# Kernel optimization log

Hardware: AMD Instinct MI355X
Metric: run time of the kernel (lower is better)

Reference implementation:

```python
import jax, jax.numpy as jnp
import numpy as np

B, C, H, W = 32, 3, 512, 512


def _make_rot(N):
    k = np.arange(N, dtype=np.float64)[None, :] * np.pi / (2 * N)
    return jnp.asarray(np.cos(k), jnp.float32), jnp.asarray(np.sin(k), jnp.float32)


def setup_inputs() -> dict:
    key = jax.random.key(0)
    X = jax.random.normal(key, (B, C, H, W), dtype=jnp.float32)
    W_r_weight, W_i_weight = _make_rot(W)
    W_r_height, W_i_height = _make_rot(H)
    return {
        "X": X,
        "W_r_weight": W_r_weight,
        "W_i_weight": W_i_weight,
        "W_r_height": W_r_height,
        "W_i_height": W_i_height,
    }


def _idct1(X, W_r, W_i):
    # 1D IDCT (DCT-III) along last axis via irfft, norm='ortho'.
    shp = X.shape
    N = shp[-1]
    Xv = X.reshape(-1, N) * 0.5
    # ortho scaling: col 0 -> *sqrt(N)*2, cols 1: -> *sqrt(N/2)*2 (after the /2)
    col_scale = np.full((N,), np.sqrt(N / 2) * 2, dtype=np.float32)
    col_scale[0] = np.sqrt(N) * 2
    Xv = Xv * jnp.asarray(col_scale)
    # V_t_i[:, 0] = 0; V_t_i[:, j] = -Xv[:, N-j] for j >= 1
    Vti = jnp.concatenate([jnp.zeros_like(Xv[:, :1]), -Xv[:, :0:-1]], axis=1)
    Vr = Xv * W_r - Vti * W_i
    Vi = Xv * W_i + Vti * W_r
    v = jnp.fft.irfft(jax.lax.complex(Vr, Vi), n=N, axis=1)  # [M, N] real
    # de-interleave: even outputs from front half, odd outputs from reversed tail
    x = jnp.zeros_like(v)
    x = x.at[:, ::2].set(v[:, : N - N // 2])
    x = x.at[:, 1::2].set(v[:, ::-1][:, : N // 2])
    return x.reshape(shp)


def reference(X, W_r_weight, W_i_weight, W_r_height, W_i_height):
    x = _idct1(X, W_r_weight, W_i_weight)          # IDCT over width
    x = jnp.swapaxes(x, -1, -2)
    x = _idct1(x, W_r_height, W_i_height)          # IDCT over height
    return jnp.swapaxes(x, -1, -2)
```

## Files before the change

kernel.cpp:

```cpp
#include <hip/hip_runtime.h>
#include <math.h>
#include <stdint.h>

#define N512 512

typedef __attribute__((ext_vector_type(8))) short short8;
typedef __attribute__((ext_vector_type(4))) float floatx4;

__device__ __forceinline__ short f2bf(float f) {
    uint32_t u = __float_as_uint(f);
    uint32_t r = u + 0x7fffu + ((u >> 16) & 1u);
    return (short)(r >> 16);
}

__device__ __forceinline__ short f2bf_fast(float f) {
    return (short)((__float_as_uint(f) + 0x8000u) >> 16);
}

__device__ __forceinline__ void gload_lds16(const void* g, void* l) {
    __builtin_amdgcn_global_load_lds(
        (const __attribute__((address_space(1))) void*)g,
        (__attribute__((address_space(3))) void*)l,
        16, 0, 0);
}

__global__ __launch_bounds__(256) void build_idct_matrix_bf16(short* __restrict__ M) {
    int idx = blockIdx.x * 256 + threadIdx.x;
    int n = idx >> 9;
    int k = idx & 511;
    int j = (k * (2 * n + 1)) & (4 * N512 - 1);
    float theta = (float)j * (3.14159265358979323846f / (2.0f * (float)N512));
    float s = (k == 0) ? 0.044194173824159216f : 0.0625f;
    M[idx] = f2bf(s * cosf(theta));
}

__global__ __launch_bounds__(256) void gemm_s1(const short* __restrict__ A,
                                               const float* __restrict__ Xg,
                                               short* __restrict__ Tg) {
    __shared__ short lds[2 * 8192];
    short* ldsA = lds;
    short* ldsB = lds + 8192;

    const int t = threadIdx.x;
    const int w = t >> 6;
    const int l = t & 63;
    const int q = (t >> 4) & 3;
    const int r = t & 15;

    const int bm0 = blockIdx.y * 128;
    const int bn0 = blockIdx.x * 128;
    const int wm0 = (w >> 1) * 64;
    const int wn0 = (w & 1) * 64;

    const float* Xs = Xg + ((long)blockIdx.z << 18);
    short* Tt = Tg + ((long)blockIdx.z << 18);

    const int rsub = l >> 3;
    const int glog = (l & 7) ^ rsub;

    const int brow = t >> 4;
    const int col4 = t & 15;
    const int bg   = col4 >> 1;
    const int bh   = col4 & 1;

    floatx4 acc[4][4] = {};

    for (int kt = 0; kt < 8; ++kt) {
        const int k0 = kt * 64;
#pragma unroll
        for (int i = 0; i < 4; ++i) {
            const int chunk = w * 4 + i;
            const int rt = chunk * 8 + rsub;
            gload_lds16(A + (((long)(bm0 + rt)) << 9) + k0 + glog * 8,
                        ldsA + chunk * 512);
        }
        {
            float4 v[8];
#pragma unroll
            for (int p = 0; p < 8; ++p) {
                const int rt = p * 16 + brow;
                v[p] = *(const float4*)(Xs + (((long)(bn0 + rt)) << 9) + k0 + col4 * 4);
            }
#pragma unroll
            for (int p = 0; p < 8; ++p) {
                const int rt = p * 16 + brow;
                const int bchunk = rt >> 3;
                const int brs = rt & 7;
                short4 o;
                o.x = f2bf_fast(v[p].x);
                o.y = f2bf_fast(v[p].y);
                o.z = f2bf_fast(v[p].z);
                o.w = f2bf_fast(v[p].w);
                *(short4*)(ldsB + bchunk * 512 + brs * 64 + ((bg ^ brs) * 8) + bh * 4) = o;
            }
        }
        __syncthreads();
#pragma unroll
        for (int kk = 0; kk < 2; ++kk) {
            const int c = kk * 4 + q;
            const int goff = ((c ^ (r & 7)) * 8);
            short8 af[4], bf[4];
#pragma unroll
            for (int i = 0; i < 4; ++i) {
                af[i] = *(const short8*)(ldsA + (wm0 + i * 16 + r) * 64 + goff);
                bf[i] = *(const short8*)(ldsB + (wn0 + i * 16 + r) * 64 + goff);
            }
#pragma unroll
            for (int i = 0; i < 4; ++i)
#pragma unroll
                for (int j = 0; j < 4; ++j)
                    acc[i][j] = __builtin_amdgcn_mfma_f32_16x16x32_bf16(
                        af[i], bf[j], acc[i][j], 0, 0, 0);
        }
        __syncthreads();
    }

#pragma unroll
    for (int i = 0; i < 4; ++i) {
        const int mrow = bm0 + wm0 + i * 16 + q * 4;
#pragma unroll
        for (int j = 0; j < 4; ++j) {
            const int ncol = bn0 + wn0 + j * 16 + r;
#pragma unroll
            for (int rg = 0; rg < 4; ++rg)
                Tt[(long)(mrow + rg) * N512 + ncol] = f2bf(acc[i][j][rg]);
        }
    }
}

__global__ __launch_bounds__(256) void gemm_s2(const short* __restrict__ A,
                                               const short* __restrict__ Bg,
                                               float* __restrict__ Cg) {
    __shared__ short lds[2 * 8192];
    short* ldsA = lds;
    short* ldsB = lds + 8192;

    const int t = threadIdx.x;
    const int w = t >> 6;
    const int l = t & 63;
    const int q = (t >> 4) & 3;
    const int r = t & 15;

    const int bm0 = blockIdx.y * 128;
    const int bn0 = blockIdx.x * 128;
    const int wm0 = (w >> 1) * 64;
    const int wn0 = (w & 1) * 64;

    const short* Bs = Bg + ((long)blockIdx.z << 18);
    float* C = Cg + ((long)blockIdx.z << 18);

    const int rsub = l >> 3;
    const int glog = (l & 7) ^ rsub;

    floatx4 acc[4][4] = {};

    for (int kt = 0; kt < 8; ++kt) {
        const int k0 = kt * 64;
#pragma unroll
        for (int i = 0; i < 4; ++i) {
            const int chunk = w * 4 + i;
            const int rt = chunk * 8 + rsub;
            gload_lds16(A + (((long)(bm0 + rt)) << 9) + k0 + glog * 8,
                        ldsA + chunk * 512);
            gload_lds16(Bs + (((long)(bn0 + rt)) << 9) + k0 + glog * 8,
                        ldsB + chunk * 512);
        }
        __syncthreads();
#pragma unroll
        for (int kk = 0; kk < 2; ++kk) {
            const int c = kk * 4 + q;
            const int goff = ((c ^ (r & 7)) * 8);
            short8 af[4], bf[4];
#pragma unroll
            for (int i = 0; i < 4; ++i) {
                af[i] = *(const short8*)(ldsA + (wm0 + i * 16 + r) * 64 + goff);
                bf[i] = *(const short8*)(ldsB + (wn0 + i * 16 + r) * 64 + goff);
            }
#pragma unroll
            for (int i = 0; i < 4; ++i)
#pragma unroll
                for (int j = 0; j < 4; ++j)
                    acc[i][j] = __builtin_amdgcn_mfma_f32_16x16x32_bf16(
                        af[i], bf[j], acc[i][j], 0, 0, 0);
        }
        __syncthreads();
    }

#pragma unroll
    for (int i = 0; i < 4; ++i) {
        const int mrow = bm0 + wm0 + i * 16 + q * 4;
#pragma unroll
        for (int j = 0; j < 4; ++j) {
            const int ncol = bn0 + wn0 + j * 16 + r;
#pragma unroll
            for (int rg = 0; rg < 4; ++rg)
                C[(long)(mrow + rg) * N512 + ncol] = acc[i][j][rg];
        }
    }
}

extern "C" void kernel_launch(void* const* d_in, const int* in_sizes, int n_in,
                              void* d_out, int out_size, void* d_ws, size_t ws_size,
                              hipStream_t stream) {
    const float* X = (const float*)d_in[0];
    float* out = (float*)d_out;

    const long plane = (long)N512 * N512;
    const int slices = in_sizes[0] / (int)plane;

    short* Mb = (short*)d_ws;
    short* Tt = Mb + plane;

    long avail = (long)ws_size - plane * 2;
    int chunk = (int)(avail / (plane * 2));
    if (chunk > slices) chunk = slices;
    if (chunk < 1) chunk = 1;

    build_idct_matrix_bf16<<<dim3((int)(plane / 256)), dim3(256), 0, stream>>>(Mb);

    for (int s0 = 0; s0 < slices; s0 += chunk) {
        int c = (s0 + chunk <= slices) ? chunk : (slices - s0);
        gemm_s1<<<dim3(4, 4, c), dim3(256), 0, stream>>>(
            Mb, X + (long)s0 * plane, Tt);
        gemm_s2<<<dim3(4, 4, c), dim3(256), 0, stream>>>(
            Mb, Tt, out + (long)s0 * plane);
    }
}
```

Baseline: 237.9 us.

## Double-buffer LDS tiles with explicit vmcnt waits in both GEMM stages

Both GEMM kernels now keep two LDS buffers and prefetch the next K-tile (global-to-LDS loads, plus register loads for the fp32 X tile in stage 1) while MFMAs run on the current tile. Hand-placed s_waitcnt vmcnt/lgkmcnt and raw barriers replace __syncthreads so loads stay in flight across compute. LDS use doubles to 64KB per block, which may cut occupancy. The host also rounds the slice chunk count down to a multiple of 32.

```diff
diff --git a/kernel.cpp b/kernel.cpp
--- a/kernel.cpp
+++ b/kernel.cpp
@@ -6,6 +6,11 @@
 
 typedef __attribute__((ext_vector_type(8))) short short8;
 typedef __attribute__((ext_vector_type(4))) float floatx4;
+
+#define VMCNT(n) asm volatile("s_waitcnt vmcnt(" #n ")" ::: "memory")
+#define LGKM0    asm volatile("s_waitcnt lgkmcnt(0)" ::: "memory")
+#define FENCE    asm volatile("" ::: "memory")
+#define BARRIER  __builtin_amdgcn_s_barrier()
 
 __device__ __forceinline__ short f2bf(float f) {
     uint32_t u = __float_as_uint(f);
@@ -37,9 +42,7 @@
 __global__ __launch_bounds__(256) void gemm_s1(const short* __restrict__ A,
                                                const float* __restrict__ Xg,
                                                short* __restrict__ Tg) {
-    __shared__ short lds[2 * 8192];
-    short* ldsA = lds;
-    short* ldsB = lds + 8192;
+    __shared__ __align__(16) short lds[4 * 8192];
 
     const int t = threadIdx.x;
     const int w = t >> 6;
@@ -64,23 +67,87 @@
     const int bh   = col4 & 1;
 
     floatx4 acc[4][4] = {};
+    float4 v[8];
+
+#pragma unroll
+    for (int p = 0; p < 8; ++p) {
+        const int rt = p * 16 + brow;
+        v[p] = *(const float4*)(Xs + (((long)(bn0 + rt)) << 9) + col4 * 4);
+    }
+#pragma unroll
+    for (int i = 0; i < 4; ++i) {
+        const int chunk = w * 4 + i;
+        const int rt = chunk * 8 + rsub;
+        gload_lds16(A + (((long)(bm0 + rt)) << 9) + glog * 8,
+                    lds + chunk * 512);
+    }
+    VMCNT(4);
+#pragma unroll
+    for (int p = 0; p < 8; ++p) {
+        const int rt = p * 16 + brow;
+        const int bchunk = rt >> 3;
+        const int brs = rt & 7;
+        short4 o;
+        o.x = f2bf_fast(v[p].x);
+        o.y = f2bf_fast(v[p].y);
+        o.z = f2bf_fast(v[p].z);
+        o.w = f2bf_fast(v[p].w);
+        *(short4*)(lds + 8192 + bchunk * 512 + brs * 64 + ((bg ^ brs) * 8) + bh * 4) = o;
+    }
+    LGKM0;
 
     for (int kt = 0; kt < 8; ++kt) {
-        const int k0 = kt * 64;
-#pragma unroll
-        for (int i = 0; i < 4; ++i) {
-            const int chunk = w * 4 + i;
-            const int rt = chunk * 8 + rsub;
-            gload_lds16(A + (((long)(bm0 + rt)) << 9) + k0 + glog * 8,
-                        ldsA + chunk * 512);
-        }
-        {
-            float4 v[8];
+        short* bufc = lds + (kt & 1) * 16384;
+        short* bufn = lds + ((kt + 1) & 1) * 16384;
+
+        if (kt < 7) {
+            const int k0n = (kt + 1) * 64;
 #pragma unroll
             for (int p = 0; p < 8; ++p) {
                 const int rt = p * 16 + brow;
-                v[p] = *(const float4*)(Xs + (((long)(bn0 + rt)) << 9) + k0 + col4 * 4);
-            }
+                v[p] = *(const float4*)(Xs + (((long)(bn0 + rt)) << 9) + k0n + col4 * 4);
+            }
+#pragma unroll
+            for (int i = 0; i < 4; ++i) {
+                const int chunk = w * 4 + i;
+                const int rt = chunk * 8 + rsub;
+                gload_lds16(A + (((long)(bm0 + rt)) << 9) + k0n + glog * 8,
+                            bufn + chunk * 512);
+            }
+            VMCNT(12);
+        } else {
+            VMCNT(0);
+        }
+        BARRIER;
+        FENCE;
+
+        {
+            short* ldsA = bufc;
+            short* ldsB = bufc + 8192;
+#pragma unroll
+            for (int kk = 0; kk < 2; ++kk) {
+                const int c = kk * 4 + q;
+                const int goff = ((c ^ (r & 7)) * 8);
+                short8 af[4], bfr[4];
+#pragma unroll
+                for (int i = 0; i < 4; ++i) {
+                    af[i]  = *(const short8*)(ldsA + (wm0 + i * 16 + r) * 64 + goff);
+                    bfr[i] = *(const short8*)(ldsB + (wn0 + i * 16 + r) * 64 + goff);
+                }
+#pragma unroll
+                for (int i = 0; i < 4; ++i)
+#pragma unroll
+                    for (int j = 0; j < 4; ++j)
+                        acc[i][j] = __builtin_amdgcn_mfma_f32_16x16x32_bf16(
+                            af[i], bfr[j], acc[i][j], 0, 0, 0);
+            }
+        }
+
+        FENCE;
+        BARRIER;
+
+        if (kt < 7) {
+            VMCNT(4);
 #pragma unroll
             for (int p = 0; p < 8; ++p) {
                 const int rt = p * 16 + brow;
@@ -91,28 +158,10 @@
                 o.y = f2bf_fast(v[p].y);
                 o.z = f2bf_fast(v[p].z);
                 o.w = f2bf_fast(v[p].w);
-                *(short4*)(ldsB + bchunk * 512 + brs * 64 + ((bg ^ brs) * 8) + bh * 4) = o;
-            }
-        }
-        __syncthreads();
-#pragma unroll
-        for (int kk = 0; kk < 2; ++kk) {
-            const int c = kk * 4 + q;
-            const int goff = ((c ^ (r & 7)) * 8);
-            short8 af[4], bf[4];
-#pragma unroll
-            for (int i = 0; i < 4; ++i) {
-                af[i] = *(const short8*)(ldsA + (wm0 + i * 16 + r) * 64 + goff);
-                bf[i] = *(const short8*)(ldsB + (wn0 + i * 16 + r) * 64 + goff);
-            }
-#pragma unroll
-            for (int i = 0; i < 4; ++i)
-#pragma unroll
-                for (int j = 0; j < 4; ++j)
-                    acc[i][j] = __builtin_amdgcn_mfma_f32_16x16x32_bf16(
-                        af[i], bf[j], acc[i][j], 0, 0, 0);
-        }
-        __syncthreads();
+                *(short4*)(bufn + 8192 + bchunk * 512 + brs * 64 + ((bg ^ brs) * 8) + bh * 4) = o;
+            }
+            LGKM0;
+        }
     }
 
 #pragma unroll
@@ -131,9 +180,7 @@
 __global__ __launch_bounds__(256) void gemm_s2(const short* __restrict__ A,
                                                const short* __restrict__ Bg,
                                                float* __restrict__ Cg) {
-    __shared__ short lds[2 * 8192];
-    short* ldsA = lds;
-    short* ldsB = lds + 8192;
+    __shared__ __align__(16) short lds[4 * 8192];
 
     const int t = threadIdx.x;
     const int w = t >> 6;
@@ -154,36 +201,62 @@
 
     floatx4 acc[4][4] = {};
 
+#pragma unroll
+    for (int i = 0; i < 4; ++i) {
+        const int chunk = w * 4 + i;
+        const int rt = chunk * 8 + rsub;
+        gload_lds16(A + (((long)(bm0 + rt)) << 9) + glog * 8,
+                    lds + chunk * 512);
+        gload_lds16(Bs + (((long)(bn0 + rt)) << 9) + glog * 8,
+                    lds + 8192 + chunk * 512);
+    }
+
     for (int kt = 0; kt < 8; ++kt) {
-        const int k0 = kt * 64;
-#pragma unroll
-        for (int i = 0; i < 4; ++i) {
-            const int chunk = w * 4 + i;
-            const int rt = chunk * 8 + rsub;
-            gload_lds16(A + (((long)(bm0 + rt)) << 9) + k0 + glog * 8,
-                        ldsA + chunk * 512);
-            gload_lds16(Bs + (((long)(bn0 + rt)) << 9) + k0 + glog * 8,
-                        ldsB + chunk * 512);
-        }
-        __syncthreads();
-#pragma unroll
-        for (int kk = 0; kk < 2; ++kk) {
-            const int c = kk * 4 + q;
-            const int goff = ((c ^ (r & 7)) * 8);
-            short8 af[4], bf[4];
+        short* bufc = lds + (kt & 1) * 16384;
+        short* bufn = lds + ((kt + 1) & 1) * 16384;
+
+        if (kt < 7) {
+            const int k0n = (kt + 1) * 64;
 #pragma unroll
             for (int i = 0; i < 4; ++i) {
-                af[i] = *(const short8*)(ldsA + (wm0 + i * 16 + r) * 64 + goff);
-                bf[i] = *(const short8*)(ldsB + (wn0 + i * 16 + r) * 64 + goff);
-            }
-#pragma unroll
-            for (int i = 0; i < 4; ++i)
-#pragma unroll
-                for (int j = 0; j < 4; ++j)
-                    acc[i][j] = __builtin_amdgcn_mfma_f32_16x16x32_bf16(
-                        af[i], bf[j], acc[i][j], 0, 0, 0);
-        }
-        __syncthreads();
+                const int chunk = w * 4 + i;
+                const int rt = chunk * 8 + rsub;
+                gload_lds16(A + (((long)(bm0 + rt)) << 9) + k0n + glog * 8,
+                            bufn + chunk * 512);
+                gload_lds16(Bs + (((long)(bn0 + rt)) << 9) + k0n + glog * 8,
+                            bufn + 8192 + chunk * 512);
+            }
+            VMCNT(8);
+        } else {
+            VMCNT(0);
+        }
+        BARRIER;
+        FENCE;
+
+        {
+            short* ldsA = bufc;
+            short* ldsB = bufc + 8192;
+#pragma unroll
+            for (int kk = 0; kk < 2; ++kk) {
+                const int c = kk * 4 + q;
+                const int goff = ((c ^ (r & 7)) * 8);
+                short8 af[4], bfr[4];
+#pragma unroll
+                for (int i = 0; i < 4; ++i) {
+                    af[i]  = *(const short8*)(ldsA + (wm0 + i * 16 + r) * 64 + goff);
+                    bfr[i] = *(const short8*)(ldsB + (wn0 + i * 16 + r) * 64 + goff);
+                }
+#pragma unroll
+                for (int i = 0; i < 4; ++i)
+#pragma unroll
+                    for (int j = 0; j < 4; ++j)
+                        acc[i][j] = __builtin_amdgcn_mfma_f32_16x16x32_bf16(
+                            af[i], bfr[j], acc[i][j], 0, 0, 0);
+            }
+        }
+
+        FENCE;
+        BARRIER;
     }
 
 #pragma unroll
@@ -214,6 +287,7 @@
     long avail = (long)ws_size - plane * 2;
     int chunk = (int)(avail / (plane * 2));
     if (chunk > slices) chunk = slices;
+    if (chunk >= 32) chunk &= ~31;
     if (chunk < 1) chunk = 1;
 
     build_idct_matrix_bf16<<<dim3((int)(plane / 256)), dim3(256), 0, stream>>>(Mb);
```

Result: faster. 232.4 us (-2.3%).

## Use single-wave 64x64 GEMM blocks without barriers and grouped tile ordering

Applied to the files above, without the earlier changes.

Both GEMM stages switch from 256-thread blocks computing 128x128 tiles to one-wave blocks computing 64x64 tiles. A flat block index is decoded so that neighbouring blocks share rows and columns of the same slice. Because each block is a single wave, __syncthreads is replaced with an explicit vmcnt(0) wait, and the stage-1 fp32 load of X is done by the same wave. The aim is to remove block-level barriers and get more independent waves in flight. The cost is that each block reuses less data, so global/L2 traffic per MFMA roughly doubles, and loads are no longer overlapped with compute.

```diff
diff --git a/kernel.cpp b/kernel.cpp
--- a/kernel.cpp
+++ b/kernel.cpp
@@ -6,6 +6,8 @@
 
 typedef __attribute__((ext_vector_type(8))) short short8;
 typedef __attribute__((ext_vector_type(4))) float floatx4;
+
+#define VMCNT0 asm volatile("s_waitcnt vmcnt(0)" ::: "memory")
 
 __device__ __forceinline__ short f2bf(float f) {
     uint32_t u = __float_as_uint(f);
@@ -22,6 +24,13 @@
         (const __attribute__((address_space(1))) void*)g,
         (__attribute__((address_space(3))) void*)l,
         16, 0, 0);
+}
+
+__device__ __forceinline__ void decode_wave(int id, int& ms, int& ps, int& z) {
+    const int g = (id >> 6) * 8 + (id & 7);
+    ms = (id >> 3) & 7;
+    ps = g & 7;
+    z  = g >> 3;
 }
 
 __global__ __launch_bounds__(256) void build_idct_matrix_bf16(short* __restrict__ M) {
@@ -34,93 +43,79 @@
     M[idx] = f2bf(s * cosf(theta));
 }
 
-__global__ __launch_bounds__(256) void gemm_s1(const short* __restrict__ A,
-                                               const float* __restrict__ Xg,
-                                               short* __restrict__ Tg) {
-    __shared__ short lds[2 * 8192];
-    short* ldsA = lds;
-    short* ldsB = lds + 8192;
-
-    const int t = threadIdx.x;
-    const int w = t >> 6;
-    const int l = t & 63;
-    const int q = (t >> 4) & 3;
-    const int r = t & 15;
-
-    const int bm0 = blockIdx.y * 128;
-    const int bn0 = blockIdx.x * 128;
-    const int wm0 = (w >> 1) * 64;
-    const int wn0 = (w & 1) * 64;
-
-    const float* Xs = Xg + ((long)blockIdx.z << 18);
-    short* Tt = Tg + ((long)blockIdx.z << 18);
+__global__ __launch_bounds__(64) void gemm_s1(const short* __restrict__ A,
+                                              const float* __restrict__ Xg,
+                                              short* __restrict__ Tg) {
+    __shared__ __align__(16) short ldsA[8 * 512];
+    __shared__ __align__(16) short ldsB[8 * 512];
+
+    const int l = threadIdx.x;
+    const int q = (l >> 4) & 3;
+    const int r = l & 15;
+
+    int ms, ps, z;
+    decode_wave(blockIdx.x, ms, ps, z);
+    const int m0 = ms * 64;
+    const int n0 = ps * 64;
+
+    const float* Xs = Xg + ((long)z << 18);
+    short* Tt = Tg + ((long)z << 18);
 
     const int rsub = l >> 3;
     const int glog = (l & 7) ^ rsub;
 
-    const int brow = t >> 4;
-    const int col4 = t & 15;
-    const int bg   = col4 >> 1;
-    const int bh   = col4 & 1;
+    const int brow = l >> 4;
 
     floatx4 acc[4][4] = {};
+    float4 v[16];
 
     for (int kt = 0; kt < 8; ++kt) {
         const int k0 = kt * 64;
 #pragma unroll
-        for (int i = 0; i < 4; ++i) {
-            const int chunk = w * 4 + i;
-            const int rt = chunk * 8 + rsub;
-            gload_lds16(A + (((long)(bm0 + rt)) << 9) + k0 + glog * 8,
-                        ldsA + chunk * 512);
-        }
-        {
-            float4 v[8];
-#pragma unroll
-            for (int p = 0; p < 8; ++p) {
-                const int rt = p * 16 + brow;
-                v[p] = *(const float4*)(Xs + (((long)(bn0 + rt)) << 9) + k0 + col4 * 4);
-            }
-#pragma unroll
-            for (int p = 0; p < 8; ++p) {
-                const int rt = p * 16 + brow;
-                const int bchunk = rt >> 3;
-                const int brs = rt & 7;
-                short4 o;
-                o.x = f2bf_fast(v[p].x);
-                o.y = f2bf_fast(v[p].y);
-                o.z = f2bf_fast(v[p].z);
-                o.w = f2bf_fast(v[p].w);
-                *(short4*)(ldsB + bchunk * 512 + brs * 64 + ((bg ^ brs) * 8) + bh * 4) = o;
-            }
-        }
-        __syncthreads();
+        for (int i = 0; i < 8; ++i)
+            gload_lds16(A + (((long)(m0 + i * 8 + rsub)) << 9) + k0 + glog * 8,
+                        ldsA + i * 512);
+#pragma unroll
+        for (int e = 0; e < 16; ++e) {
+            const int rt = e * 4 + brow;
+            v[e] = *(const float4*)(Xs + (((long)(n0 + rt)) << 9) + k0 + r * 4);
+        }
+        VMCNT0;
+#pragma unroll
+        for (int e = 0; e < 16; ++e) {
+            const int rt = e * 4 + brow;
+            short4 o;
+            o.x = f2bf_fast(v[e].x);
+            o.y = f2bf_fast(v[e].y);
+            o.z = f2bf_fast(v[e].z);
+            o.w = f2bf_fast(v[e].w);
+            *(short4*)(ldsB + rt * 64 + (((r >> 1) ^ (rt & 7)) * 8) + (r & 1) * 4) = o;
+        }
 #pragma unroll
         for (int kk = 0; kk < 2; ++kk) {
             const int c = kk * 4 + q;
             const int goff = ((c ^ (r & 7)) * 8);
-            short8 af[4], bf[4];
+            short8 af[4], bfr[4];
 #pragma unroll
             for (int i = 0; i < 4; ++i) {
-                af[i] = *(const short8*)(ldsA + (wm0 + i * 16 + r) * 64 + goff);
-                bf[i] = *(const short8*)(ldsB + (wn0 + i * 16 + r) * 64 + goff);
+                af[i]  = *(const short8*)(ldsA + (i * 16 + r) * 64 + goff);
+                bfr[i] = *(const short8*)(ldsB + (i * 16 + r) * 64 + goff);
             }
 #pragma unroll
             for (int i = 0; i < 4; ++i)
 #pragma unroll
                 for (int j = 0; j < 4; ++j)
                     acc[i][j] = __builtin_amdgcn_mfma_f32_16x16x32_bf16(
-                        af[i], bf[j], acc[i][j], 0, 0, 0);
-        }
-        __syncthreads();
+                        af[i], bfr[j], acc[i][j], 0, 0, 0);
+        }
     }
 
 #pragma unroll
     for (int i = 0; i < 4; ++i) {
-        const int mrow = bm0 + wm0 + i * 16 + q * 4;
+        const int mrow = m0 + i * 16 + q * 4;
 #pragma unroll
         for (int j = 0; j < 4; ++j) {
-            const int ncol = bn0 + wn0 + j * 16 + r;
+            const int ncol = n0 + j * 16 + r;
 #pragma unroll
             for (int rg = 0; rg < 4; ++rg)
                 Tt[(long)(mrow + rg) * N512 + ncol] = f2bf(acc[i][j][rg]);
@@ -128,26 +123,23 @@
     }
 }
 
-__global__ __launch_bounds__(256) void gemm_s2(const short* __restrict__ A,
-                                               const short* __restrict__ Bg,
-                                               float* __restrict__ Cg) {
-    __shared__ short lds[2 * 8192];
-    short* ldsA = lds;
-    short* ldsB = lds + 8192;
-
-    const int t = threadIdx.x;
-    const int w = t >> 6;
-    const int l = t & 63;
-    const int q = (t >> 4) & 3;
-    const int r = t & 15;
-
-    const int bm0 = blockIdx.y * 128;
-    const int bn0 = blockIdx.x * 128;
-    const int wm0 = (w >> 1) * 64;
-    const int wn0 = (w & 1) * 64;
-
-    const short* Bs = Bg + ((long)blockIdx.z << 18);
-    float* C = Cg + ((long)blockIdx.z << 18);
+__global__ __launch_bounds__(64) void gemm_s2(const short* __restrict__ A,
+                                              const short* __restrict__ Bg,
+                                              float* __restrict__ Cg) {
+    __shared__ __align__(16) short ldsA[8 * 512];
+    __shared__ __align__(16) short ldsB[8 * 512];
+
+    const int l = threadIdx.x;
+    const int q = (l >> 4) & 3;
+    const int r = l & 15;
+
+    int ms, ps, z;
+    decode_wave(blockIdx.x, ms, ps, z);
+    const int m0 = ms * 64;
+    const int n0 = ps * 64;
+
+    const short* Bs = Bg + ((long)z << 18);
+    float* C = Cg + ((long)z << 18);
 
     const int rsub = l >> 3;
     const int glog = (l & 7) ^ rsub;
@@ -157,41 +149,38 @@
     for (int kt = 0; kt < 8; ++kt) {
         const int k0 = kt * 64;
 #pragma unroll
-        for (int i = 0; i < 4; ++i) {
-            const int chunk = w * 4 + i;
-            const int rt = chunk * 8 + rsub;
-            gload_lds16(A + (((long)(bm0 + rt)) << 9) + k0 + glog * 8,
-                        ldsA + chunk * 512);
-            gload_lds16(Bs + (((long)(bn0 + rt)) << 9) + k0 + glog * 8,
-                        ldsB + chunk * 512);
-        }
-        __syncthreads();
+        for (int i = 0; i < 8; ++i) {
+            gload_lds16(A + (((long)(m0 + i * 8 + rsub)) << 9) + k0 + glog * 8,
+                        ldsA + i * 512);
+            gload_lds16(Bs + (((long)(n0 + i * 8 + rsub)) << 9) + k0 + glog * 8,
+                        ldsB + i * 512);
+        }
+        VMCNT0;
 #pragma unroll
         for (int kk = 0; kk < 2; ++kk) {
             const int c = kk * 4 + q;
             const int goff = ((c ^ (r & 7)) * 8);
-            short8 af[4], bf[4];
+            short8 af[4], bfr[4];
 #pragma unroll
             for (int i = 0; i < 4; ++i) {
-                af[i] = *(const short8*)(ldsA + (wm0 + i * 16 + r) * 64 + goff);
-                bf[i] = *(const short8*)(ldsB + (wn0 + i * 16 + r) * 64 + goff);
+                af[i]  = *(const short8*)(ldsA + (i * 16 + r) * 64 + goff);
+                bfr[i] = *(const short8*)(ldsB + (i * 16 + r) * 64 + goff);
             }
 #pragma unroll
             for (int i = 0; i < 4; ++i)
 #pragma unroll
                 for (int j = 0; j < 4; ++j)
                     acc[i][j] = __builtin_amdgcn_mfma_f32_16x16x32_bf16(
-                        af[i], bf[j], acc[i][j], 0, 0, 0);
-        }
-        __syncthreads();
+                        af[i], bfr[j], acc[i][j], 0, 0, 0);
+        }
     }
 
 #pragma unroll
     for (int i = 0; i < 4; ++i) {
-        const int mrow = bm0 + wm0 + i * 16 + q * 4;
+        const int mrow = m0 + i * 16 + q * 4;
 #pragma unroll
         for (int j = 0; j < 4; ++j) {
-            const int ncol = bn0 + wn0 + j * 16 + r;
+            const int ncol = n0 + j * 16 + r;
 #pragma unroll
             for (int rg = 0; rg < 4; ++rg)
                 C[(long)(mrow + rg) * N512 + ncol] = acc[i][j][rg];
@@ -220,9 +209,9 @@
 
     for (int s0 = 0; s0 < slices; s0 += chunk) {
         int c = (s0 + chunk <= slices) ? chunk : (slices - s0);
-        gemm_s1<<<dim3(4, 4, c), dim3(256), 0, stream>>>(
+        gemm_s1<<<dim3(64 * c), dim3(64), 0, stream>>>(
             Mb, X + (long)s0 * plane, Tt);
-        gemm_s2<<<dim3(4, 4, c), dim3(256), 0, stream>>>(
+        gemm_s2<<<dim3(64 * c), dim3(64), 0, stream>>>(
             Mb, Tt, out + (long)s0 * plane);
     }
 }
```

Result: slower. 259.1 us (+8.9%).

## Exploit IDCT matrix even/odd symmetry to halve GEMM MACs in both stages

Applied to the files above, without the earlier changes.

Splits the 512x512 IDCT basis into even-k and odd-k halves and uses the symmetry M[511-n][k] = (-1)^k M[n][k]. Each output row pair n and 511-n is then formed from two half-size products (P+Q and P-Q), which halves the MFMA work and the reads of the basis matrix. The intermediate is stored de-interleaved by parity so stage two can load the even and odd halves directly. The cost is twice the LDS per block (64KB), half as many blocks, and scattered epilogue stores. An explicit vmcnt wait is also added before the LDS writes and barriers.

```diff
diff --git a/kernel.cpp b/kernel.cpp
--- a/kernel.cpp
+++ b/kernel.cpp
@@ -6,6 +6,8 @@
 
 typedef __attribute__((ext_vector_type(8))) short short8;
 typedef __attribute__((ext_vector_type(4))) float floatx4;
+
+#define VMCNT0 asm volatile("s_waitcnt vmcnt(0)" ::: "memory")
 
 __device__ __forceinline__ short f2bf(float f) {
     uint32_t u = __float_as_uint(f);
@@ -24,177 +26,226 @@
         16, 0, 0);
 }
 
-__global__ __launch_bounds__(256) void build_idct_matrix_bf16(short* __restrict__ M) {
+__global__ __launch_bounds__(256) void build_idct_matrix_bf16(short* __restrict__ Mb) {
     int idx = blockIdx.x * 256 + threadIdx.x;
-    int n = idx >> 9;
-    int k = idx & 511;
-    int j = (k * (2 * n + 1)) & (4 * N512 - 1);
-    float theta = (float)j * (3.14159265358979323846f / (2.0f * (float)N512));
+    int par = idx >> 16;
+    int e = idx & 65535;
+    int n = e >> 8;
+    int j = e & 255;
+    int k = 2 * j + par;
+    int jr = (k * (2 * n + 1)) & (4 * N512 - 1);
+    float theta = (float)jr * (3.14159265358979323846f / (2.0f * (float)N512));
     float s = (k == 0) ? 0.044194173824159216f : 0.0625f;
-    M[idx] = f2bf(s * cosf(theta));
-}
-
-__global__ __launch_bounds__(256) void gemm_s1(const short* __restrict__ A,
+    Mb[par * 65536 + n * 256 + j] = f2bf(s * cosf(theta));
+}
+
+__global__ __launch_bounds__(256) void gemm_s1(const short* __restrict__ Mb,
                                                const float* __restrict__ Xg,
                                                short* __restrict__ Tg) {
-    __shared__ short lds[2 * 8192];
-    short* ldsA = lds;
-    short* ldsB = lds + 8192;
+    __shared__ __align__(16) short lds[32768];
+    short* ldsAe = lds;
+    short* ldsAo = lds + 8192;
+    short* ldsBe = lds + 16384;
+    short* ldsBo = lds + 24576;
 
     const int t = threadIdx.x;
     const int w = t >> 6;
     const int l = t & 63;
-    const int q = (t >> 4) & 3;
-    const int r = t & 15;
-
+    const int q = (l >> 4) & 3;
+    const int r = l & 15;
+
+    const int bn0 = blockIdx.x * 128;
     const int bm0 = blockIdx.y * 128;
-    const int bn0 = blockIdx.x * 128;
     const int wm0 = (w >> 1) * 64;
     const int wn0 = (w & 1) * 64;
 
     const float* Xs = Xg + ((long)blockIdx.z << 18);
-    short* Tt = Tg + ((long)blockIdx.z << 18);
+    short* Te = Tg + ((long)blockIdx.z << 18);
+
+    const short* Me = Mb;
+    const short* Mo = Mb + 65536;
 
     const int rsub = l >> 3;
     const int glog = (l & 7) ^ rsub;
 
     const int brow = t >> 4;
-    const int col4 = t & 15;
-    const int bg   = col4 >> 1;
-    const int bh   = col4 & 1;
-
-    floatx4 acc[4][4] = {};
-
-    for (int kt = 0; kt < 8; ++kt) {
+    const int bcol = t & 15;
+    const int bg = bcol >> 1;
+    const int bh = bcol & 1;
+
+    floatx4 accP[4][4] = {};
+    floatx4 accQ[4][4] = {};
+
+    for (int kt = 0; kt < 4; ++kt) {
         const int k0 = kt * 64;
 #pragma unroll
         for (int i = 0; i < 4; ++i) {
-            const int chunk = w * 4 + i;
-            const int rt = chunk * 8 + rsub;
-            gload_lds16(A + (((long)(bm0 + rt)) << 9) + k0 + glog * 8,
-                        ldsA + chunk * 512);
-        }
-        {
-            float4 v[8];
-#pragma unroll
-            for (int p = 0; p < 8; ++p) {
-                const int rt = p * 16 + brow;
-                v[p] = *(const float4*)(Xs + (((long)(bn0 + rt)) << 9) + k0 + col4 * 4);
-            }
-#pragma unroll
-            for (int p = 0; p < 8; ++p) {
-                const int rt = p * 16 + brow;
-                const int bchunk = rt >> 3;
-                const int brs = rt & 7;
-                short4 o;
-                o.x = f2bf_fast(v[p].x);
-                o.y = f2bf_fast(v[p].y);
-                o.z = f2bf_fast(v[p].z);
-                o.w = f2bf_fast(v[p].w);
-                *(short4*)(ldsB + bchunk * 512 + brs * 64 + ((bg ^ brs) * 8) + bh * 4) = o;
-            }
+            const int ch = w * 4 + i;
+            const int arow = bm0 + ch * 8 + rsub;
+            gload_lds16(Me + arow * 256 + k0 + glog * 8, ldsAe + ch * 512);
+            gload_lds16(Mo + arow * 256 + k0 + glog * 8, ldsAo + ch * 512);
+        }
+        float4 va[8], vb[8];
+#pragma unroll
+        for (int p = 0; p < 8; ++p) {
+            const int row = bn0 + p * 16 + brow;
+            const float* base = Xs + ((long)row << 9) + kt * 128 + bcol * 8;
+            va[p] = *(const float4*)(base);
+            vb[p] = *(const float4*)(base + 4);
+        }
+        VMCNT0;
+#pragma unroll
+        for (int p = 0; p < 8; ++p) {
+            const int rt = p * 16 + brow;
+            short4 ev, od;
+            ev.x = f2bf_fast(va[p].x); ev.y = f2bf_fast(va[p].z);
+            ev.z = f2bf_fast(vb[p].x); ev.w = f2bf_fast(vb[p].z);
+            od.x = f2bf_fast(va[p].y); od.y = f2bf_fast(va[p].w);
+            od.z = f2bf_fast(vb[p].y); od.w = f2bf_fast(vb[p].w);
+            const int addr = rt * 64 + ((bg ^ (rt & 7)) * 8) + bh * 4;
+            *(short4*)(ldsBe + addr) = ev;
+            *(short4*)(ldsBo + addr) = od;
         }
         __syncthreads();
 #pragma unroll
         for (int kk = 0; kk < 2; ++kk) {
             const int c = kk * 4 + q;
             const int goff = ((c ^ (r & 7)) * 8);
-            short8 af[4], bf[4];
-#pragma unroll
-            for (int i = 0; i < 4; ++i) {
-                af[i] = *(const short8*)(ldsA + (wm0 + i * 16 + r) * 64 + goff);
-                bf[i] = *(const short8*)(ldsB + (wn0 + i * 16 + r) * 64 + goff);
-            }
-#pragma unroll
-            for (int i = 0; i < 4; ++i)
-#pragma unroll
-                for (int j = 0; j < 4; ++j)
-                    acc[i][j] = __builtin_amdgcn_mfma_f32_16x16x32_bf16(
-                        af[i], bf[j], acc[i][j], 0, 0, 0);
+            short8 af[4], bf4[4];
+#pragma unroll
+            for (int i = 0; i < 4; ++i) {
+                af[i]  = *(const short8*)(ldsAe + (wm0 + i * 16 + r) * 64 + goff);
+                bf4[i] = *(const short8*)(ldsBe + (wn0 + i * 16 + r) * 64 + goff);
+            }
+#pragma unroll
+            for (int i = 0; i < 4; ++i)
+#pragma unroll
+                for (int j = 0; j < 4; ++j)
+                    accP[i][j] = __builtin_amdgcn_mfma_f32_16x16x32_bf16(
+                        af[i], bf4[j], accP[i][j], 0, 0, 0);
+#pragma unroll
+            for (int i = 0; i < 4; ++i) {
+                af[i]  = *(const short8*)(ldsAo + (wm0 + i * 16 + r) * 64 + goff);
+                bf4[i] = *(const short8*)(ldsBo + (wn0 + i * 16 + r) * 64 + goff);
+            }
+#pragma unroll
+            for (int i = 0; i < 4; ++i)
+#pragma unroll
+                for (int j = 0; j < 4; ++j)
+                    accQ[i][j] = __builtin_amdgcn_mfma_f32_16x16x32_bf16(
+                        af[i], bf4[j], accQ[i][j], 0, 0, 0);
         }
         __syncthreads();
     }
 
 #pragma unroll
     for (int i = 0; i < 4; ++i) {
-        const int mrow = bm0 + wm0 + i * 16 + q * 4;
+        const int nb = bm0 + wm0 + i * 16 + q * 4;
 #pragma unroll
         for (int j = 0; j < 4; ++j) {
-            const int ncol = bn0 + wn0 + j * 16 + r;
-#pragma unroll
-            for (int rg = 0; rg < 4; ++rg)
-                Tt[(long)(mrow + rg) * N512 + ncol] = f2bf(acc[i][j][rg]);
-        }
-    }
-}
-
-__global__ __launch_bounds__(256) void gemm_s2(const short* __restrict__ A,
-                                               const short* __restrict__ Bg,
+            const int h = bn0 + wn0 + j * 16 + r;
+            short* dst = Te + (h & 1) * 131072 + (h >> 1);
+#pragma unroll
+            for (int rg = 0; rg < 4; ++rg) {
+                const int n = nb + rg;
+                const float p = accP[i][j][rg], qq = accQ[i][j][rg];
+                dst[n * 256] = f2bf(p + qq);
+                dst[(511 - n) * 256] = f2bf(p - qq);
+            }
+        }
+    }
+}
+
+__global__ __launch_bounds__(256) void gemm_s2(const short* __restrict__ Mb,
+                                               const short* __restrict__ Tg,
                                                float* __restrict__ Cg) {
-    __shared__ short lds[2 * 8192];
-    short* ldsA = lds;
-    short* ldsB = lds + 8192;
+    __shared__ __align__(16) short lds[32768];
+    short* ldsAe = lds;
+    short* ldsAo = lds + 8192;
+    short* ldsBe = lds + 16384;
+    short* ldsBo = lds + 24576;
 
     const int t = threadIdx.x;
     const int w = t >> 6;
     const int l = t & 63;
-    const int q = (t >> 4) & 3;
-    const int r = t & 15;
-
+    const int q = (l >> 4) & 3;
+    const int r = l & 15;
+
+    const int bn0 = blockIdx.x * 128;
     const int bm0 = blockIdx.y * 128;
-    const int bn0 = blockIdx.x * 128;
     const int wm0 = (w >> 1) * 64;
     const int wn0 = (w & 1) * 64;
 
-    const short* Bs = Bg + ((long)blockIdx.z << 18);
+    const short* Te = Tg + ((long)blockIdx.z << 18);
     float* C = Cg + ((long)blockIdx.z << 18);
+
+    const short* Me = Mb;
+    const short* Mo = Mb + 65536;
 
     const int rsub = l >> 3;
     const int glog = (l & 7) ^ rsub;
 
-    floatx4 acc[4][4] = {};
-
-    for (int kt = 0; kt < 8; ++kt) {
+    floatx4 accR[4][4] = {};
+    floatx4 accS[4][4] = {};
+
+    for (int kt = 0; kt < 4; ++kt) {
         const int k0 = kt * 64;
 #pragma unroll
         for (int i = 0; i < 4; ++i) {
-            const int chunk = w * 4 + i;
-            const int rt = chunk * 8 + rsub;
-            gload_lds16(A + (((long)(bm0 + rt)) << 9) + k0 + glog * 8,
-                        ldsA + chunk * 512);
-            gload_lds16(Bs + (((long)(bn0 + rt)) << 9) + k0 + glog * 8,
-                        ldsB + chunk * 512);
-        }
+            const int ch = w * 4 + i;
+            const int arow = bm0 + ch * 8 + rsub;
+            const int brw  = bn0 + ch * 8 + rsub;
+            gload_lds16(Me + arow * 256 + k0 + glog * 8, ldsAe + ch * 512);
+            gload_lds16(Mo + arow * 256 + k0 + glog * 8, ldsAo + ch * 512);
+            gload_lds16(Te + brw * 256 + k0 + glog * 8, ldsBe + ch * 512);
+            gload_lds16(Te + 131072 + brw * 256 + k0 + glog * 8, ldsBo + ch * 512);
+        }
+        VMCNT0;
         __syncthreads();
 #pragma unroll
         for (int kk = 0; kk < 2; ++kk) {
             const int c = kk * 4 + q;
             const int goff = ((c ^ (r & 7)) * 8);
-            short8 af[4], bf[4];
-#pragma unroll
-            for (int i = 0; i < 4; ++i) {
-                af[i] = *(const short8*)(ldsA + (wm0 + i * 16 + r) * 64 + goff);
-                bf[i] = *(const short8*)(ldsB + (wn0 + i * 16 + r) * 64 + goff);
-            }
-#pragma unroll
-            for (int i = 0; i < 4; ++i)
-#pragma unroll
-                for (int j = 0; j < 4; ++j)
-                    acc[i][j] = __builtin_amdgcn_mfma_f32_16x16x32_bf16(
-                        af[i], bf[j], acc[i][j], 0, 0, 0);
+            short8 af[4], bf4[4];
+#pragma unroll
+            for (int i = 0; i < 4; ++i) {
+                af[i]  = *(const short8*)(ldsAe + (wm0 + i * 16 + r) * 64 + goff);
+                bf4[i] = *(const short8*)(ldsBe + (wn0 + i * 16 + r) * 64 + goff);
+            }
+#pragma unroll
+            for (int i = 0; i < 4; ++i)
+#pragma unroll
+                for (int j = 0; j < 4; ++j)
+                    accR[i][j] = __builtin_amdgcn_mfma_f32_16x16x32_bf16(
+                        af[i], bf4[j], accR[i][j], 0, 0, 0);
+#pragma unroll
+            for (int i = 0; i < 4; ++i) {
+                af[i]  = *(const short8*)(ldsAo + (wm0 + i * 16 + r) * 64 + goff);
+                bf4[i] = *(const short8*)(ldsBo + (wn0 + i * 16 + r) * 64 + goff);
+            }
+#pragma unroll
+            for (int i = 0; i < 4; ++i)
+#pragma unroll
+                for (int j = 0; j < 4; ++j)
+                    accS[i][j] = __builtin_amdgcn_mfma_f32_16x16x32_bf16(
+                        af[i], bf4[j], accS[i][j], 0, 0, 0);
         }
         __syncthreads();
     }
 
 #pragma unroll
     for (int i = 0; i < 4; ++i) {
-        const int mrow = bm0 + wm0 + i * 16 + q * 4;
+        const int mb = bm0 + wm0 + i * 16 + q * 4;
 #pragma unroll
         for (int j = 0; j < 4; ++j) {
-            const int ncol = bn0 + wn0 + j * 16 + r;
-#pragma unroll
-            for (int rg = 0; rg < 4; ++rg)
-                C[(long)(mrow + rg) * N512 + ncol] = acc[i][j][rg];
+            const int n = bn0 + wn0 + j * 16 + r;
+#pragma unroll
+            for (int rg = 0; rg < 4; ++rg) {
+                const int m = mb + rg;
+                const float rr = accR[i][j][rg], ss = accS[i][j][rg];
+                C[(long)m * N512 + n] = rr + ss;
+                C[(long)(511 - m) * N512 + n] = rr - ss;
+            }
         }
     }
 }
@@ -209,20 +260,20 @@
     const int slices = in_sizes[0] / (int)plane;
 
     short* Mb = (short*)d_ws;
-    short* Tt = Mb + plane;
-
-    long avail = (long)ws_size - plane * 2;
+    short* Tt = Mb + 131072;
+
+    long avail = (long)ws_size - 262144;
     int chunk = (int)(avail / (plane * 2));
     if (chunk > slices) chunk = slices;
     if (chunk < 1) chunk = 1;
 
-    build_idct_matrix_bf16<<<dim3((int)(plane / 256)), dim3(256), 0, stream>>>(Mb);
+    build_idct_matrix_bf16<<<dim3(512), dim3(256), 0, stream>>>(Mb);
 
     for (int s0 = 0; s0 < slices; s0 += chunk) {
         int c = (s0 + chunk <= slices) ? chunk : (slices - s0);
-        gemm_s1<<<dim3(4, 4, c), dim3(256), 0, stream>>>(
+        gemm_s1<<<dim3(4, 2, c), dim3(256), 0, stream>>>(
             Mb, X + (long)s0 * plane, Tt);
-        gemm_s2<<<dim3(4, 4, c), dim3(256), 0, stream>>>(
+        gemm_s2<<<dim3(4, 2, c), dim3(256), 0, stream>>>(
             Mb, Tt, out + (long)s0 * plane);
     }
 }
```

New measurement: 253.5 us. 1.07x slower.
